# Performance work log

Hardware: AMD Instinct MI355X
Metric: run time of the kernel (lower is better)

## Reference

```python
import jax, jax.numpy as jnp
import numpy as np

B, N = 2, 512
CS, CZ = 384, 128
H, D, P, PV = 12, 16, 4, 8
W_C = (2.0 / (9.0 * P)) ** 0.5
W_L = (1.0 / 3.0) ** 0.5
CAT = H * CZ + H * D + H * PV * 3 + H * PV  # concat width into output linear


def setup_inputs() -> dict:
    key = jax.random.key(0)
    ks = jax.random.split(key, 14)
    sc = lambda n: np.float32(1.0 / np.sqrt(n))
    s_i = jax.random.normal(ks[0], (B, N, CS), jnp.float32)
    z_ij = jax.random.normal(ks[1], (B, N, N, CZ), jnp.float32)
    rots = jax.random.normal(ks[2], (B, N, 3, 3), jnp.float32)
    trans = jax.random.normal(ks[3], (B, N, 3), jnp.float32)
    wq = jax.random.normal(ks[4], (CS, H, D), jnp.float32) * sc(CS)
    wk = jax.random.normal(ks[5], (CS, H, D), jnp.float32) * sc(CS)
    wv = jax.random.normal(ks[6], (CS, H, D), jnp.float32) * sc(CS)
    wqp = jax.random.normal(ks[7], (CS, H, P, 3), jnp.float32) * sc(CS)
    wkp = jax.random.normal(ks[8], (CS, H, P, 3), jnp.float32) * sc(CS)
    wvp = jax.random.normal(ks[9], (CS, H, PV, 3), jnp.float32) * sc(CS)
    wb = jax.random.normal(ks[10], (CZ, H), jnp.float32) * sc(CZ)
    gamma = jax.random.normal(ks[11], (H,), jnp.float32)
    wout = jax.random.normal(ks[12], (CAT, CS), jnp.float32) * sc(CAT)
    bout = jnp.zeros((CS,), jnp.float32)
    return dict(s_i=s_i, z_ij=z_ij, rots=rots, trans=trans, wq=wq, wk=wk, wv=wv,
                wqp=wqp, wkp=wkp, wvp=wvp, wb=wb, gamma=gamma, wout=wout, bout=bout)


def reference(s_i, z_ij, rots, trans, wq, wk, wv, wqp, wkp, wvp, wb, gamma, wout, bout):
    # rigid apply: x_global = R @ x_local + t, per residue, broadcast over (h, p)
    def rig_apply(x):  # x: (b,i,h,p,3)
        return jnp.einsum('bixy,bihpy->bihpx', rots, x) + trans[:, :, None, None, :]

    def rig_invert_apply(x):  # R^T @ (x - t)
        return jnp.einsum('biyx,bihpy->bihpx', rots, x - trans[:, :, None, None, :])

    q = jnp.einsum('bic,chd->bihd', s_i, wq)
    k = jnp.einsum('bic,chd->bihd', s_i, wk)
    v = jnp.einsum('bic,chd->bihd', s_i, wv)
    qp = jnp.einsum('bic,chpx->bihpx', s_i, wqp)
    kp = jnp.einsum('bic,chpx->bihpx', s_i, wkp)
    vp = jnp.einsum('bic,chpx->bihpx', s_i, wvp)

    b_ij = jnp.einsum('bijc,ch->bijh', z_ij, wb)  # pair bias

    tq = rig_apply(qp)  # (b,i,h,p,3) in global frame
    tk = rig_apply(kp)
    # squared point distances summed over points: (b,i,j,h)
    d2 = jnp.sum((tq[:, :, None] - tk[:, None]) ** 2, axis=(-1, -2))

    a_s = jnp.einsum('bihd,bjhd->bijh', q, k) * np.float32(1.0 / np.sqrt(D))
    logits = W_L * (a_s + b_ij - (W_C * 0.5) * gamma * d2)
    a = jax.nn.softmax(logits, axis=2)  # softmax over j (dim=-2 of bijh)

    o_hat = jnp.einsum('bijh,bijd->bihd', a, z_ij)   # pair-value aggregation
    o = jnp.einsum('bijh,bjhd->bihd', a, v)          # scalar values
    tv = rig_apply(vp)                               # point values in global frame
    o_hp = rig_invert_apply(jnp.einsum('bijh,bjhpx->bihpx', a, tv))
    o_hp_norm = jnp.sqrt(jnp.sum(o_hp ** 2, axis=-1))  # (b,i,h,p)

    cat = jnp.concatenate([
        o_hat.reshape(B, N, H * CZ),
        o.reshape(B, N, H * D),
        o_hp.reshape(B, N, H * PV * 3),
        o_hp_norm.reshape(B, N, H * PV),
    ], axis=-1)
    return cat @ wout + bout
```

## Files before the change

### kernel.cpp

```cpp
#include <hip/hip_runtime.h>
#include <hip/hip_bf16.h>
#include <math.h>

#define BB 2
#define NN 512
#define CS 384
#define CZ 128
#define HH 12
#define CATW 2112

#define W_L_CONST 0.57735026919f
#define W_C_HALF 0.11785113019f
#define INV_SQRT_D 0.25f
#define LGP 516

__global__ void k_proj(const float* __restrict__ s_i,
                       const float* __restrict__ rots,
                       const float* __restrict__ trans,
                       const float* __restrict__ wq,
                       const float* __restrict__ wk,
                       const float* __restrict__ wv,
                       const float* __restrict__ wqp,
                       const float* __restrict__ wkp,
                       const float* __restrict__ wvp,
                       float* __restrict__ qw, float* __restrict__ kw,
                       float* __restrict__ vw, float* __restrict__ tqw,
                       float* __restrict__ tkw, float* __restrict__ tvw) {
  int t0 = blockIdx.x * 2;
  __shared__ float s_row[2][CS];
  __shared__ float praw[2][576];
  __shared__ float R[2][9], T[2][3];
  int tid = threadIdx.x;
  for (int idx = tid; idx < 2 * CS; idx += 256) {
    int tok = idx / CS, c = idx % CS;
    s_row[tok][c] = s_i[(size_t)(t0 + tok) * CS + c];
  }
  if (tid < 18) R[tid / 9][tid % 9] = rots[t0 * 9 + tid];
  if (tid < 6) T[tid / 3][tid % 3] = trans[t0 * 3 + tid];
  __syncthreads();

  for (int f = tid; f < 1152; f += 256) {
    const float* wp;
    int stride;
    if (f < 576) {
      int sel = f / 192, r = f % 192;
      wp = ((sel == 0) ? wq : (sel == 1) ? wk : wv) + r;
      stride = 192;
    } else {
      int g = f - 576;
      if (g < 144)      { wp = wqp + g;        stride = 144; }
      else if (g < 288) { wp = wkp + (g - 144); stride = 144; }
      else              { wp = wvp + (g - 288); stride = 288; }
    }
    float a0 = 0.f, a1 = 0.f;
    #pragma unroll 8
    for (int c = 0; c < CS; c++) {
      float w = wp[(size_t)c * stride];
      a0 += s_row[0][c] * w;
      a1 += s_row[1][c] * w;
    }
    if (f < 576) {
      int sel = f / 192, r = f % 192;
      float* dst = (sel == 0) ? qw : (sel == 1) ? kw : vw;
      dst[(size_t)(t0 + 0) * 192 + r] = a0;
      dst[(size_t)(t0 + 1) * 192 + r] = a1;
    } else {
      int g = f - 576;
      praw[0][g] = a0;
      praw[1][g] = a1;
    }
  }
  __syncthreads();
  for (int idx = tid; idx < 1152; idx += 256) {
    int tok = idx / 576, f = idx % 576;
    int base, r;
    float* dst;
    if (f < 144)      { r = f;       base = 0;   dst = tqw + (size_t)(t0 + tok) * 144; }
    else if (f < 288) { r = f - 144; base = 144; dst = tkw + (size_t)(t0 + tok) * 144; }
    else              { r = f - 288; base = 288; dst = tvw + (size_t)(t0 + tok) * 288; }
    int hp = r / 3, x = r % 3;
    float v0 = praw[tok][base + hp * 3 + 0];
    float v1 = praw[tok][base + hp * 3 + 1];
    float v2 = praw[tok][base + hp * 3 + 2];
    dst[r] = R[tok][x * 3 + 0] * v0 + R[tok][x * 3 + 1] * v1 + R[tok][x * 3 + 2] * v2 + T[tok][x];
  }
}

__global__ void k_bias(const float* __restrict__ z,
                       const float* __restrict__ wb,
                       float* __restrict__ bw) {
  __shared__ float zt[64][129];
  __shared__ float wbs[CZ * HH];
  __shared__ float bbs[64][12];
  int tid = threadIdx.x;
  int r0 = blockIdx.x * 64;
  int bi = r0 >> 9, j0 = r0 & 511;

  for (int idx = tid; idx < CZ * HH; idx += 256) wbs[idx] = wb[idx];
  const float* zbase = z + (size_t)r0 * CZ;
  for (int s = 0; s < 8; s++) {
    int idx = tid + s * 256;
    int row = idx >> 5, q = idx & 31;
    float4 v = *(const float4*)(zbase + (size_t)row * CZ + q * 4);
    zt[row][q * 4 + 0] = v.x;
    zt[row][q * 4 + 1] = v.y;
    zt[row][q * 4 + 2] = v.z;
    zt[row][q * 4 + 3] = v.w;
  }
  __syncthreads();

  int row = tid & 63, hbase = tid >> 6;
  float a0 = 0.f, a1 = 0.f, a2 = 0.f;
  #pragma unroll 8
  for (int c = 0; c < CZ; c++) {
    float zv = zt[row][c];
    a0 += zv * wbs[c * HH + hbase];
    a1 += zv * wbs[c * HH + hbase + 4];
    a2 += zv * wbs[c * HH + hbase + 8];
  }
  bbs[row][hbase] = a0;
  bbs[row][hbase + 4] = a1;
  bbs[row][hbase + 8] = a2;
  __syncthreads();

  for (int idx = tid; idx < 768; idx += 256) {
    int h = idx / 64, jl = idx % 64;
    bw[((size_t)bi * HH + h) * NN + j0 + jl] = bbs[jl][h];
  }
}

__global__ void k_att(const float* __restrict__ qw,
                      const float* __restrict__ kw,
                      const float* __restrict__ tqw,
                      const float* __restrict__ tkw,
                      const float* __restrict__ vw,
                      const float* __restrict__ tvw,
                      const float* __restrict__ gamma,
                      const float* __restrict__ rots,
                      const float* __restrict__ trans,
                      float* __restrict__ bw,
                      float* __restrict__ catm) {
  int bi = blockIdx.x;
  int b = bi / NN;
  __shared__ float lg[HH][LGP];
  __shared__ float qrow[192], tqrow[144], gam[HH];
  __shared__ float rm[HH][4], rs[HH][4];
  __shared__ float praw[288], ohp[288], R[9], T[3];
  int tid = threadIdx.x;
  int lane = tid & 63, wid = tid >> 6;

  const float* bwrow = bw + (size_t)bi * (HH * NN);
  for (int idx = tid; idx < HH * NN; idx += 256) {
    int h = idx >> 9, j = idx & 511;
    lg[h][j] = bwrow[idx];
  }
  for (int idx = tid; idx < 192; idx += 256) qrow[idx] = qw[(size_t)bi * 192 + idx];
  if (tid < 144) tqrow[tid] = tqw[(size_t)bi * 144 + tid];
  if (tid < HH) gam[tid] = gamma[tid];
  if (tid >= 16 && tid < 25) R[tid - 16] = rots[bi * 9 + (tid - 16)];
  if (tid >= 32 && tid < 35) T[tid - 32] = trans[bi * 3 + (tid - 32)];
  __syncthreads();

  for (int s = 0; s < 24; s++) {
    int task = tid + s * 256;
    int j = task / 12, h = task % 12;
    const float4* kd = (const float4*)(kw + ((size_t)(b * NN + j)) * 192 + h * 16);
    float as = 0.f;
    #pragma unroll
    for (int q = 0; q < 4; q++) {
      float4 kv = kd[q];
      as += qrow[h * 16 + q * 4 + 0] * kv.x + qrow[h * 16 + q * 4 + 1] * kv.y +
            qrow[h * 16 + q * 4 + 2] * kv.z + qrow[h * 16 + q * 4 + 3] * kv.w;
    }
    const float4* td = (const float4*)(tkw + ((size_t)(b * NN + j)) * 144 + h * 12);
    float d2 = 0.f;
    #pragma unroll
    for (int q = 0; q < 3; q++) {
      float4 tv = td[q];
      float d0 = tqrow[h * 12 + q * 4 + 0] - tv.x;
      float d1 = tqrow[h * 12 + q * 4 + 1] - tv.y;
      float d2_ = tqrow[h * 12 + q * 4 + 2] - tv.z;
      float d3 = tqrow[h * 12 + q * 4 + 3] - tv.w;
      d2 += d0 * d0 + d1 * d1 + d2_ * d2_ + d3 * d3;
    }
    lg[h][j] = W_L_CONST * (as * INV_SQRT_D + lg[h][j] - W_C_HALF * gam[h] * d2);
  }
  __syncthreads();

  #pragma unroll
  for (int h = 0; h < HH; h++) {
    float m = fmaxf(lg[h][tid], lg[h][tid + 256]);
    #pragma unroll
    for (int off = 32; off >= 1; off >>= 1) m = fmaxf(m, __shfl_xor(m, off, 64));
    if (lane == 0) rm[h][wid] = m;
  }
  __syncthreads();
  #pragma unroll
  for (int h = 0; h < HH; h++) {
    float mx = fmaxf(fmaxf(rm[h][0], rm[h][1]), fmaxf(rm[h][2], rm[h][3]));
    float e0 = __expf(lg[h][tid] - mx);
    float e1 = __expf(lg[h][tid + 256] - mx);
    lg[h][tid] = e0;
    lg[h][tid + 256] = e1;
    float s = e0 + e1;
    #pragma unroll
    for (int off = 32; off >= 1; off >>= 1) s += __shfl_xor(s, off, 64);
    if (lane == 0) rs[h][wid] = s;
  }
  __syncthreads();
  #pragma unroll
  for (int h = 0; h < HH; h++) {
    float inv = 1.0f / (rs[h][0] + rs[h][1] + rs[h][2] + rs[h][3]);
    lg[h][tid] *= inv;
    lg[h][tid + 256] *= inv;
  }
  __syncthreads();

  float* awrow = bw + (size_t)bi * (HH * NN);
  for (int idx = tid; idx < HH * NN; idx += 256) {
    int j = idx / 12, h = idx % 12;
    awrow[idx] = lg[h][j];
  }

  float* crow = catm + (size_t)bi * CATW;
  for (int task = tid; task < 480; task += 256) {
    if (task < 192) {
      int h = task / 16;
      const float* vp = vw + (size_t)b * NN * 192 + task;
      float sum = 0.f;
      #pragma unroll 4
      for (int j = 0; j < NN; j++) sum += lg[h][j] * vp[(size_t)j * 192];
      crow[1536 + task] = sum;
    } else {
      int f = task - 192;
      int h = f / 24;
      const float* tp = tvw + (size_t)b * NN * 288 + f;
      float sum = 0.f;
      #pragma unroll 4
      for (int j = 0; j < NN; j++) sum += lg[h][j] * tp[(size_t)j * 288];
      praw[f] = sum;
    }
  }
  __syncthreads();
  for (int f = tid; f < 288; f += 256) {
    int g = f / 3, x = f % 3;
    float v0 = praw[g * 3 + 0] - T[0];
    float v1 = praw[g * 3 + 1] - T[1];
    float v2 = praw[g * 3 + 2] - T[2];
    float val = R[0 * 3 + x] * v0 + R[1 * 3 + x] * v1 + R[2 * 3 + x] * v2;
    ohp[f] = val;
    crow[1728 + f] = val;
  }
  __syncthreads();
  if (tid < 96) {
    float x0 = ohp[tid * 3 + 0];
    float x1 = ohp[tid * 3 + 1];
    float x2 = ohp[tid * 3 + 2];
    crow[2016 + tid] = sqrtf(x0 * x0 + x1 * x1 + x2 * x2);
  }
}

__global__ void k_ohat(const float* __restrict__ z,
                       const float* __restrict__ aw,
                       float* __restrict__ catm) {
  int bi = blockIdx.x;
  __shared__ float buf[HH * NN];
  int tid = threadIdx.x;
  const float* awrow = aw + (size_t)bi * (HH * NN);
  for (int idx = tid; idx < HH * NN; idx += 256) buf[idx] = awrow[idx];
  __syncthreads();

  int c0 = (tid & 63) * 2, jg = tid >> 6;
  const float* zrow = z + ((size_t)bi * NN + jg * 128) * CZ;
  float accx[HH], accy[HH];
  #pragma unroll
  for (int h = 0; h < HH; h++) { accx[h] = 0.f; accy[h] = 0.f; }

  for (int jj = 0; jj < 128; jj++) {
    float2 zv = *(const float2*)(zrow + (size_t)jj * CZ + c0);
    const float4* ap = (const float4*)(buf + (jg * 128 + jj) * 12);
    float4 A0 = ap[0], A1 = ap[1], A2 = ap[2];
    accx[0] += A0.x * zv.x;  accy[0] += A0.x * zv.y;
    accx[1] += A0.y * zv.x;  accy[1] += A0.y * zv.y;
    accx[2] += A0.z * zv.x;  accy[2] += A0.z * zv.y;
    accx[3] += A0.w * zv.x;  accy[3] += A0.w * zv.y;
    accx[4] += A1.x * zv.x;  accy[4] += A1.x * zv.y;
    accx[5] += A1.y * zv.x;  accy[5] += A1.y * zv.y;
    accx[6] += A1.z * zv.x;  accy[6] += A1.z * zv.y;
    accx[7] += A1.w * zv.x;  accy[7] += A1.w * zv.y;
    accx[8] += A2.x * zv.x;  accy[8] += A2.x * zv.y;
    accx[9] += A2.y * zv.x;  accy[9] += A2.y * zv.y;
    accx[10] += A2.z * zv.x; accy[10] += A2.z * zv.y;
    accx[11] += A2.w * zv.x; accy[11] += A2.w * zv.y;
  }
  __syncthreads();
  #pragma unroll
  for (int h = 0; h < HH; h++) {
    buf[jg * 1536 + h * CZ + c0] = accx[h];
    buf[jg * 1536 + h * CZ + c0 + 1] = accy[h];
  }
  __syncthreads();
  float* crow = catm + (size_t)bi * CATW;
  #pragma unroll
  for (int s = 0; s < 6; s++) {
    int out = tid + s * 256;
    crow[out] = buf[out] + buf[1536 + out] + buf[3072 + out] + buf[4608 + out];
  }
}

__global__ void k_gemm(const float* __restrict__ catm,
                       const float* __restrict__ wout,
                       const float* __restrict__ bout,
                       float* __restrict__ out) {
  __shared__ float As[32][33], Bs[32][33];
  int tid = threadIdx.x;
  int tx = tid % 32, ty = tid / 32;
  int row0 = blockIdx.y * 32, col0 = blockIdx.x * 32;
  float acc[4] = {0.f, 0.f, 0.f, 0.f};
  for (int kt = 0; kt < CATW / 32; kt++) {
    #pragma unroll
    for (int s = 0; s < 4; s++)
      As[ty + 8 * s][tx] = catm[(size_t)(row0 + ty + 8 * s) * CATW + kt * 32 + tx];
    #pragma unroll
    for (int s = 0; s < 4; s++)
      Bs[ty + 8 * s][tx] = wout[(size_t)(kt * 32 + ty + 8 * s) * 384 + col0 + tx];
    __syncthreads();
    #pragma unroll
    for (int kk = 0; kk < 32; kk++) {
      float bv = Bs[kk][tx];
      #pragma unroll
      for (int s = 0; s < 4; s++) acc[s] += As[ty + 8 * s][kk] * bv;
    }
    __syncthreads();
  }
  float bias = bout[col0 + tx];
  #pragma unroll
  for (int s = 0; s < 4; s++)
    out[(size_t)(row0 + ty + 8 * s) * 384 + col0 + tx] = acc[s] + bias;
}

extern "C" void kernel_launch(void* const* d_in, const int* in_sizes, int n_in,
                              void* d_out, int out_size, void* d_ws, size_t ws_size,
                              hipStream_t stream) {
  const float* s_i   = (const float*)d_in[0];
  const float* z     = (const float*)d_in[1];
  const float* rots  = (const float*)d_in[2];
  const float* trans = (const float*)d_in[3];
  const float* wq    = (const float*)d_in[4];
  const float* wk    = (const float*)d_in[5];
  const float* wv    = (const float*)d_in[6];
  const float* wqp   = (const float*)d_in[7];
  const float* wkp   = (const float*)d_in[8];
  const float* wvp   = (const float*)d_in[9];
  const float* wb    = (const float*)d_in[10];
  const float* gamma = (const float*)d_in[11];
  const float* wout  = (const float*)d_in[12];
  const float* bout  = (const float*)d_in[13];
  float* out = (float*)d_out;

  float* ws = (float*)d_ws;
  const size_t TOK = (size_t)BB * NN;
  float* qw  = ws;
  float* kw  = qw + TOK * 192;
  float* vw  = kw + TOK * 192;
  float* tqw = vw + TOK * 192;
  float* tkw = tqw + TOK * 144;
  float* tvw = tkw + TOK * 144;
  float* bw  = tvw + TOK * 288;
  float* catm = bw + TOK * HH * NN;

  k_proj<<<BB * NN / 2, 256, 0, stream>>>(s_i, rots, trans, wq, wk, wv, wqp, wkp, wvp,
                                          qw, kw, vw, tqw, tkw, tvw);
  k_bias<<<BB * NN * NN / 64, 256, 0, stream>>>(z, wb, bw);
  k_att<<<BB * NN, 256, 0, stream>>>(qw, kw, tqw, tkw, vw, tvw, gamma, rots, trans,
                                     bw, catm);
  k_ohat<<<BB * NN, 256, 0, stream>>>(z, bw, catm);
  dim3 g(384 / 32, 1024 / 32);
  k_gemm<<<g, 256, 0, stream>>>(catm, wout, bout, out);
}
```

Baseline: 862.0 us.

## Fuse pair-value aggregation into attention kernel and split-K the output GEMM

Merges the o_hat aggregation over z into the attention kernel, so the softmax weights are used straight from shared memory instead of being written to global and read back by a separate kernel. The scalar and point value aggregation is reworked so each wave covers a quarter of j, with partial sums reduced through shared memory. The output GEMM moves to 64x64 register tiles with 4-way split-K plus a separate reduction kernel that adds the bias. In exchange there is more shared memory and register pressure in the attention kernel, an extra launch and a partial-output buffer.

```diff
diff --git a/kernel.cpp b/kernel.cpp
--- a/kernel.cpp
+++ b/kernel.cpp
@@ -129,7 +129,8 @@
   }
 }
 
-__global__ void k_att(const float* __restrict__ qw,
+__global__ void k_att(const float* __restrict__ z,
+                      const float* __restrict__ qw,
                       const float* __restrict__ kw,
                       const float* __restrict__ tqw,
                       const float* __restrict__ tkw,
@@ -138,11 +139,12 @@
                       const float* __restrict__ gamma,
                       const float* __restrict__ rots,
                       const float* __restrict__ trans,
-                      float* __restrict__ bw,
+                      const float* __restrict__ bw,
                       float* __restrict__ catm) {
   int bi = blockIdx.x;
   int b = bi / NN;
   __shared__ float lg[HH][LGP];
+  __shared__ float opart[4][480];
   __shared__ float qrow[192], tqrow[144], gam[HH];
   __shared__ float rm[HH][4], rs[HH][4];
   __shared__ float praw[288], ohp[288], R[9], T[3];
@@ -150,15 +152,13 @@
   int lane = tid & 63, wid = tid >> 6;
 
   const float* bwrow = bw + (size_t)bi * (HH * NN);
-  for (int idx = tid; idx < HH * NN; idx += 256) {
-    int h = idx >> 9, j = idx & 511;
-    lg[h][j] = bwrow[idx];
-  }
+  for (int idx = tid; idx < HH * NN; idx += 256)
+    lg[idx >> 9][idx & 511] = bwrow[idx];
   for (int idx = tid; idx < 192; idx += 256) qrow[idx] = qw[(size_t)bi * 192 + idx];
   if (tid < 144) tqrow[tid] = tqw[(size_t)bi * 144 + tid];
   if (tid < HH) gam[tid] = gamma[tid];
-  if (tid >= 16 && tid < 25) R[tid - 16] = rots[bi * 9 + (tid - 16)];
-  if (tid >= 32 && tid < 35) T[tid - 32] = trans[bi * 3 + (tid - 32)];
+  if (tid < 9) R[tid] = rots[bi * 9 + tid];
+  if (tid < 3) T[tid] = trans[bi * 3 + tid];
   __syncthreads();
 
   for (int s = 0; s < 24; s++) {
@@ -216,30 +216,29 @@
   }
   __syncthreads();
 
-  float* awrow = bw + (size_t)bi * (HH * NN);
-  for (int idx = tid; idx < HH * NN; idx += 256) {
-    int j = idx / 12, h = idx % 12;
-    awrow[idx] = lg[h][j];
-  }
-
   float* crow = catm + (size_t)bi * CATW;
-  for (int task = tid; task < 480; task += 256) {
-    if (task < 192) {
-      int h = task / 16;
-      const float* vp = vw + (size_t)b * NN * 192 + task;
-      float sum = 0.f;
-      #pragma unroll 4
-      for (int j = 0; j < NN; j++) sum += lg[h][j] * vp[(size_t)j * 192];
-      crow[1536 + task] = sum;
-    } else {
-      int f = task - 192;
-      int h = f / 24;
-      const float* tp = tvw + (size_t)b * NN * 288 + f;
-      float sum = 0.f;
-      #pragma unroll 4
-      for (int j = 0; j < NN; j++) sum += lg[h][j] * tp[(size_t)j * 288];
-      praw[f] = sum;
-    }
+  int j0 = wid * 128;
+
+  for (int t = lane; t < 480; t += 64) {
+    const float* src;
+    int h, str;
+    if (t < 192) { h = t >> 4; src = vw + (size_t)b * NN * 192 + t; str = 192; }
+    else { int f = t - 192; h = f / 24; src = tvw + (size_t)b * NN * 288 + f; str = 288; }
+    float sum = 0.f;
+    for (int jj = 0; jj < 128; jj += 4) {
+      float4 av = *(const float4*)&lg[h][j0 + jj];
+      sum += av.x * src[(size_t)(j0 + jj + 0) * str]
+           + av.y * src[(size_t)(j0 + jj + 1) * str]
+           + av.z * src[(size_t)(j0 + jj + 2) * str]
+           + av.w * src[(size_t)(j0 + jj + 3) * str];
+    }
+    opart[wid][t] = sum;
+  }
+  __syncthreads();
+  for (int t = tid; t < 480; t += 256) {
+    float s = opart[0][t] + opart[1][t] + opart[2][t] + opart[3][t];
+    if (t < 192) crow[1536 + t] = s;
+    else praw[t - 192] = s;
   }
   __syncthreads();
   for (int f = tid; f < 288; f += 256) {
@@ -258,85 +257,93 @@
     float x2 = ohp[tid * 3 + 2];
     crow[2016 + tid] = sqrtf(x0 * x0 + x1 * x1 + x2 * x2);
   }
-}
-
-__global__ void k_ohat(const float* __restrict__ z,
-                       const float* __restrict__ aw,
-                       float* __restrict__ catm) {
-  int bi = blockIdx.x;
-  __shared__ float buf[HH * NN];
-  int tid = threadIdx.x;
-  const float* awrow = aw + (size_t)bi * (HH * NN);
-  for (int idx = tid; idx < HH * NN; idx += 256) buf[idx] = awrow[idx];
-  __syncthreads();
-
-  int c0 = (tid & 63) * 2, jg = tid >> 6;
-  const float* zrow = z + ((size_t)bi * NN + jg * 128) * CZ;
-  float accx[HH], accy[HH];
-  #pragma unroll
-  for (int h = 0; h < HH; h++) { accx[h] = 0.f; accy[h] = 0.f; }
-
-  for (int jj = 0; jj < 128; jj++) {
-    float2 zv = *(const float2*)(zrow + (size_t)jj * CZ + c0);
-    const float4* ap = (const float4*)(buf + (jg * 128 + jj) * 12);
-    float4 A0 = ap[0], A1 = ap[1], A2 = ap[2];
-    accx[0] += A0.x * zv.x;  accy[0] += A0.x * zv.y;
-    accx[1] += A0.y * zv.x;  accy[1] += A0.y * zv.y;
-    accx[2] += A0.z * zv.x;  accy[2] += A0.z * zv.y;
-    accx[3] += A0.w * zv.x;  accy[3] += A0.w * zv.y;
-    accx[4] += A1.x * zv.x;  accy[4] += A1.x * zv.y;
-    accx[5] += A1.y * zv.x;  accy[5] += A1.y * zv.y;
-    accx[6] += A1.z * zv.x;  accy[6] += A1.z * zv.y;
-    accx[7] += A1.w * zv.x;  accy[7] += A1.w * zv.y;
-    accx[8] += A2.x * zv.x;  accy[8] += A2.x * zv.y;
-    accx[9] += A2.y * zv.x;  accy[9] += A2.y * zv.y;
-    accx[10] += A2.z * zv.x; accy[10] += A2.z * zv.y;
-    accx[11] += A2.w * zv.x; accy[11] += A2.w * zv.y;
+
+  int hw = lane >> 5, c4 = (lane & 31) * 4;
+  float4 acc[HH];
+  #pragma unroll
+  for (int h = 0; h < HH; h++) acc[h] = make_float4(0.f, 0.f, 0.f, 0.f);
+  for (int stp = 0; stp < 64; stp++) {
+    int j = j0 + stp * 2 + hw;
+    float4 zv = *(const float4*)(z + ((size_t)bi * NN + j) * CZ + c4);
+    #pragma unroll
+    for (int h = 0; h < HH; h++) {
+      float a = lg[h][j];
+      acc[h].x += a * zv.x;
+      acc[h].y += a * zv.y;
+      acc[h].z += a * zv.z;
+      acc[h].w += a * zv.w;
+    }
   }
   __syncthreads();
   #pragma unroll
   for (int h = 0; h < HH; h++) {
-    buf[jg * 1536 + h * CZ + c0] = accx[h];
-    buf[jg * 1536 + h * CZ + c0 + 1] = accy[h];
-  }
-  __syncthreads();
-  float* crow = catm + (size_t)bi * CATW;
+    acc[h].x += __shfl_xor(acc[h].x, 32, 64);
+    acc[h].y += __shfl_xor(acc[h].y, 32, 64);
+    acc[h].z += __shfl_xor(acc[h].z, 32, 64);
+    acc[h].w += __shfl_xor(acc[h].w, 32, 64);
+  }
+  float* pbuf = &lg[0][0];
+  if (lane < 32) {
+    #pragma unroll
+    for (int h = 0; h < HH; h++)
+      *(float4*)&pbuf[wid * 1536 + h * 128 + lane * 4] = acc[h];
+  }
+  __syncthreads();
   #pragma unroll
   for (int s = 0; s < 6; s++) {
-    int out = tid + s * 256;
-    crow[out] = buf[out] + buf[1536 + out] + buf[3072 + out] + buf[4608 + out];
-  }
-}
-
+    int idx = tid + s * 256;
+    crow[idx] = pbuf[idx] + pbuf[1536 + idx] + pbuf[3072 + idx] + pbuf[4608 + idx];
+  }
+}
+
+#define KCH 528
 __global__ void k_gemm(const float* __restrict__ catm,
                        const float* __restrict__ wout,
-                       const float* __restrict__ bout,
-                       float* __restrict__ out) {
-  __shared__ float As[32][33], Bs[32][33];
+                       float* __restrict__ pout) {
+  __shared__ float As[16][68];
+  __shared__ float Bs[16][64];
   int tid = threadIdx.x;
-  int tx = tid % 32, ty = tid / 32;
-  int row0 = blockIdx.y * 32, col0 = blockIdx.x * 32;
-  float acc[4] = {0.f, 0.f, 0.f, 0.f};
-  for (int kt = 0; kt < CATW / 32; kt++) {
-    #pragma unroll
-    for (int s = 0; s < 4; s++)
-      As[ty + 8 * s][tx] = catm[(size_t)(row0 + ty + 8 * s) * CATW + kt * 32 + tx];
-    #pragma unroll
-    for (int s = 0; s < 4; s++)
-      Bs[ty + 8 * s][tx] = wout[(size_t)(kt * 32 + ty + 8 * s) * 384 + col0 + tx];
+  int n0 = blockIdx.x * 64, m0 = blockIdx.y * 64, kbase = blockIdx.z * KCH;
+  int tx = tid & 15, ty = tid >> 4;
+  int sm = tid & 63, skk4 = tid >> 6;
+  int bkk = tid >> 4, bn4 = (tid & 15) * 4;
+  float acc[4][4] = {};
+  for (int kt = 0; kt < KCH / 16; kt++) {
+    int k0 = kbase + kt * 16;
+    float4 ga = *(const float4*)(catm + (size_t)(m0 + sm) * CATW + k0 + skk4 * 4);
+    float4 gb = *(const float4*)(wout + (size_t)(k0 + bkk) * 384 + n0 + bn4);
     __syncthreads();
-    #pragma unroll
-    for (int kk = 0; kk < 32; kk++) {
-      float bv = Bs[kk][tx];
-      #pragma unroll
-      for (int s = 0; s < 4; s++) acc[s] += As[ty + 8 * s][kk] * bv;
-    }
+    As[skk4 * 4 + 0][sm] = ga.x;
+    As[skk4 * 4 + 1][sm] = ga.y;
+    As[skk4 * 4 + 2][sm] = ga.z;
+    As[skk4 * 4 + 3][sm] = ga.w;
+    *(float4*)&Bs[bkk][bn4] = gb;
     __syncthreads();
-  }
-  float bias = bout[col0 + tx];
-  #pragma unroll
-  for (int s = 0; s < 4; s++)
-    out[(size_t)(row0 + ty + 8 * s) * 384 + col0 + tx] = acc[s] + bias;
+    #pragma unroll
+    for (int kk = 0; kk < 16; kk++) {
+      float4 av = *(const float4*)&As[kk][ty * 4];
+      float4 bv = *(const float4*)&Bs[kk][tx * 4];
+      acc[0][0] += av.x * bv.x; acc[0][1] += av.x * bv.y; acc[0][2] += av.x * bv.z; acc[0][3] += av.x * bv.w;
+      acc[1][0] += av.y * bv.x; acc[1][1] += av.y * bv.y; acc[1][2] += av.y * bv.z; acc[1][3] += av.y * bv.w;
+      acc[2][0] += av.z * bv.x; acc[2][1] += av.z * bv.y; acc[2][2] += av.z * bv.z; acc[2][3] += av.z * bv.w;
+      acc[3][0] += av.w * bv.x; acc[3][1] += av.w * bv.y; acc[3][2] += av.w * bv.z; acc[3][3] += av.w * bv.w;
+    }
+  }
+  float* pdst = pout + (size_t)blockIdx.z * (1024 * 384);
+  #pragma unroll
+  for (int mm = 0; mm < 4; mm++) {
+    *(float4*)&pdst[(size_t)(m0 + ty * 4 + mm) * 384 + n0 + tx * 4] =
+        make_float4(acc[mm][0], acc[mm][1], acc[mm][2], acc[mm][3]);
+  }
+}
+
+__global__ void k_red(const float* __restrict__ pout,
+                      const float* __restrict__ bout,
+                      float* __restrict__ out) {
+  int idx = blockIdx.x * 256 + threadIdx.x;
+  const int TOTAL = 1024 * 384;
+  float s = pout[idx] + pout[TOTAL + idx] + pout[2 * TOTAL + idx] + pout[3 * TOTAL + idx];
+  out[idx] = s + bout[idx % 384];
 }
 
 extern "C" void kernel_launch(void* const* d_in, const int* in_sizes, int n_in,
@@ -368,13 +375,14 @@
   float* tvw = tkw + TOK * 144;
   float* bw  = tvw + TOK * 288;
   float* catm = bw + TOK * HH * NN;
+  float* pout = catm + TOK * CATW;
 
   k_proj<<<BB * NN / 2, 256, 0, stream>>>(s_i, rots, trans, wq, wk, wv, wqp, wkp, wvp,
                                           qw, kw, vw, tqw, tkw, tvw);
   k_bias<<<BB * NN * NN / 64, 256, 0, stream>>>(z, wb, bw);
-  k_att<<<BB * NN, 256, 0, stream>>>(qw, kw, tqw, tkw, vw, tvw, gamma, rots, trans,
+  k_att<<<BB * NN, 256, 0, stream>>>(z, qw, kw, tqw, tkw, vw, tvw, gamma, rots, trans,
                                      bw, catm);
-  k_ohat<<<BB * NN, 256, 0, stream>>>(z, bw, catm);
-  dim3 g(384 / 32, 1024 / 32);
-  k_gemm<<<g, 256, 0, stream>>>(catm, wout, bout, out);
-}
+  dim3 gg(6, 16, 4);
+  k_gemm<<<gg, 256, 0, stream>>>(catm, wout, pout);
+  k_red<<<(1024 * 384) / 256, 256, 0, stream>>>(pout, bout, out);
+}
```

Result: faster. 704.4 us (-18.3%).
